# Kernel optimization log

Hardware: AMD Instinct MI355X
Metric: run time of the kernel (lower is better)

The kernel has to match this reference:

```python
import jax, jax.numpy as jnp
import numpy as np

EPS = 1e-5

def layernorm(x, g, b):
    mu = jnp.mean(x, axis=-1, keepdims=True)
    var = jnp.mean(jnp.square(x - mu), axis=-1, keepdims=True)
    return (x - mu) * jax.lax.rsqrt(var + EPS) * g + b

def setup_inputs() -> dict:
    key = jax.random.key(0)
    B, C, W = 1, 256, 64           # C = x_h_dim = query_dim
    D = 256                        # inner_dim = heads(1) * dim_head(256)
    ks = jax.random.split(key, 32)
    sc = 0.02
    inp = {
        'x': jax.random.normal(ks[0], (B, C, W, W), jnp.float32),
        'h': jax.random.normal(ks[1], (B, C, W, W), jnp.float32),
        's': jax.random.normal(ks[2], (B, C, W, W), jnp.float32),
        'm': jax.random.normal(ks[3], (B, C, W, W), jnp.float32),
        't': jax.random.normal(ks[4], (B, C), jnp.float32),
        'wt': jax.random.normal(ks[5], (C, D), jnp.float32) * sc,
        'bt': jnp.zeros((D,), jnp.float32),
        'wk_x': jax.random.normal(ks[6], (C, D), jnp.float32) * sc,
        'wv_x': jax.random.normal(ks[7], (C, D), jnp.float32) * sc,
        'g_x': jnp.ones((C,), jnp.float32), 'be_x': jnp.zeros((C,), jnp.float32),
        'wk_h': jax.random.normal(ks[8], (C, D), jnp.float32) * sc,
        'wv_h': jax.random.normal(ks[9], (C, D), jnp.float32) * sc,
        'g_h': jnp.ones((C,), jnp.float32), 'be_h': jnp.zeros((C,), jnp.float32),
        'wk_s': jax.random.normal(ks[10], (C, D), jnp.float32) * sc,
        'wv_s': jax.random.normal(ks[11], (C, D), jnp.float32) * sc,
        'g_s': jnp.ones((C,), jnp.float32), 'be_s': jnp.zeros((C,), jnp.float32),
        'wk_m': jax.random.normal(ks[12], (C, D), jnp.float32) * sc,
        'wv_m': jax.random.normal(ks[13], (C, D), jnp.float32) * sc,
        'g_m': jnp.ones((C,), jnp.float32), 'be_m': jnp.zeros((C,), jnp.float32),
        'w_geglu': jax.random.normal(ks[14], (D, 2 * D), jnp.float32) * sc,
        'b_geglu': jnp.zeros((2 * D,), jnp.float32),
        'w_ff2': jax.random.normal(ks[15], (D, D), jnp.float32) * sc,
        'b_ff2': jnp.zeros((D,), jnp.float32),
        'g_res': jnp.ones((D,), jnp.float32), 'be_res': jnp.zeros((D,), jnp.float32),
        'w_out': jax.random.normal(ks[16], (D, C), jnp.float32) * sc,
        'b_out': jnp.zeros((C,), jnp.float32),
        'imageWidth': W,
    }
    return inp

def reference(x, h, s, m, t, wt, bt, wk_x, wv_x, g_x, be_x, wk_h, wv_h, g_h, be_h,
              wk_s, wv_s, g_s, be_s, wk_m, wv_m, g_m, be_m,
              w_geglu, b_geglu, w_ff2, b_ff2, g_res, be_res, w_out, b_out, imageWidth):
    B, C, W, _ = x.shape
    N = W * W
    D = wt.shape[1]
    scale = 1.0 / jnp.sqrt(jnp.float32(D))  # dim_head**-0.5 (heads=1)

    # query: t_transform(t) broadcast over all spatial positions -> [B, N, D]
    q = t @ wt + bt
    query = jnp.broadcast_to(q[:, None, :], (B, N, D))

    def tokens(a):  # b c h w -> b (h w) c
        return a.reshape(B, C, N).transpose(0, 2, 1)

    mods = []
    for a, g, be, wk, wv in ((x, g_x, be_x, wk_x, wv_x), (h, g_h, be_h, wk_h, wv_h),
                             (s, g_s, be_s, wk_s, wv_s), (m, g_m, be_m, wk_m, wv_m)):
        a = layernorm(tokens(a), g, be)
        mods.append((a @ wk, a @ wv))  # (k, v) each [B, N, D]

    sims = [jnp.einsum('bid,bjd->bij', query, k) * scale for k, _ in mods]
    combined = jnp.concatenate(sims, axis=-1)          # [B, N, 4N]
    attn = jax.nn.softmax(combined, axis=-1)
    parts = jnp.split(attn, 4, axis=-1)

    out = sum(jnp.einsum('bij,bjd->bid', a, v) for a, (_, v) in zip(parts, mods))

    # FeedForward(inner_dim, mult=1, glu=True) on layernormed sum
    r = layernorm(out, g_res, be_res)
    gg = r @ w_geglu + b_geglu
    u, gate = jnp.split(gg, 2, axis=-1)
    ff = (u * jax.nn.gelu(gate, approximate=False)) @ w_ff2 + b_ff2

    y = ff @ w_out + b_out                              # [B, N, C]
    return y.transpose(0, 2, 1).reshape(B, C, W, W)
```

## Files before the change

### kernel.cpp

```cpp
#include <hip/hip_runtime.h>
#include <math.h>

#define N_TOK 4096

#define OFF_Q     0
#define OFF_GU    256
#define OFF_GUBU  1280
#define OFF_SIM   2048
#define OFF_MU    18432
#define OFF_RINV  34816
#define OFF_BLK   51200
#define OFF_SOFT  51248
#define OFF_W     51264
#define OFF_OUTV  52288
#define OFF_R     52544
#define OFF_GG    52800
#define OFF_FF    53312
#define OFF_Y     53568

__global__ void kInit(const float* __restrict__ bt, const float* __restrict__ b_geglu,
                      const float* __restrict__ b_ff2, const float* __restrict__ b_out,
                      float* __restrict__ ws) {
  const int tid = threadIdx.x;
  ws[OFF_GG + tid] = b_geglu[tid];
  if (tid < 256) {
    ws[OFF_Q + tid] = bt[tid];
    ws[OFF_OUTV + tid] = 0.0f;
    ws[OFF_FF + tid] = b_ff2[tid];
    ws[OFF_Y + tid] = b_out[tid];
  }
  if (tid < 8) ws[OFF_GUBU + tid] = 0.0f;
}

__global__ void kQ(const float* __restrict__ t, const float* __restrict__ wt,
                   float* __restrict__ ws) {
  const int tid = threadIdx.x;
  const int c0 = blockIdx.x * 16;
  float acc = 0.f;
  #pragma unroll
  for (int i = 0; i < 16; ++i) {
    int c = c0 + i;
    acc += t[c] * wt[c * 256 + tid];
  }
  atomicAdd(&ws[OFF_Q + tid], acc);
}

__global__ void kU(const float* __restrict__ wk0, const float* __restrict__ wk1,
                   const float* __restrict__ wk2, const float* __restrict__ wk3,
                   const float* __restrict__ g0, const float* __restrict__ g1,
                   const float* __restrict__ g2, const float* __restrict__ g3,
                   const float* __restrict__ be0, const float* __restrict__ be1,
                   const float* __restrict__ be2, const float* __restrict__ be3,
                   float* __restrict__ ws) {
  const int b = blockIdx.x;
  const int m = b >> 3;
  const int c0 = (b & 7) * 32;
  const int tid = threadIdx.x;
  const int w = tid >> 6, lane = tid & 63;
  const float* wk = (m == 0) ? wk0 : (m == 1) ? wk1 : (m == 2) ? wk2 : wk3;
  const float* g  = (m == 0) ? g0  : (m == 1) ? g1  : (m == 2) ? g2  : g3;
  const float* be = (m == 0) ? be0 : (m == 1) ? be1 : (m == 2) ? be2 : be3;

  __shared__ float qsh[256];
  __shared__ float red[8];
  qsh[tid] = ws[OFF_Q + tid];
  __syncthreads();
  const float4 qv = ((const float4*)qsh)[lane];

  float lGU = 0.f, lBU = 0.f;
  #pragma unroll
  for (int r = 0; r < 8; ++r) {
    int c = c0 + w * 8 + r;
    float4 w4 = ((const float4*)(wk + c * 256))[lane];
    float s = w4.x * qv.x + w4.y * qv.y + w4.z * qv.z + w4.w * qv.w;
    for (int o = 32; o > 0; o >>= 1) s += __shfl_down(s, o, 64);
    if (lane == 0) {
      float u = s;
      float gu = g[c] * u;
      ws[OFF_GU + m * 256 + c] = gu;
      lGU += gu;
      lBU += be[c] * u;
    }
  }
  if (lane == 0) { red[w] = lGU; red[4 + w] = lBU; }
  __syncthreads();
  if (tid == 0) {
    atomicAdd(&ws[OFF_GUBU + m], red[0] + red[1] + red[2] + red[3]);
    atomicAdd(&ws[OFF_GUBU + 4 + m], red[4] + red[5] + red[6] + red[7]);
  }
}

__global__ void kB(const float* __restrict__ A0, const float* __restrict__ A1,
                   const float* __restrict__ A2, const float* __restrict__ A3,
                   float* __restrict__ ws) {
  const int b = blockIdx.x;
  const int m = b >> 6;
  const int jbase = (b & 63) * 64;
  const int tid = threadIdx.x;
  const int l = tid & 63;
  const int qq = tid >> 6;
  const float* A = (m == 0) ? A0 : (m == 1) ? A1 : (m == 2) ? A2 : A3;

  __shared__ float gu[256];
  __shared__ float p1[256], p2[256], p3[256];
  gu[tid] = ws[OFF_GU + m * 256 + tid];
  __syncthreads();

  float s1 = 0.f, s2 = 0.f, s3 = 0.f;
  const float* Abase = A + jbase + l;
  #pragma unroll 8
  for (int i = 0; i < 64; ++i) {
    int c = qq * 64 + i;
    float v = Abase[c * N_TOK];
    s1 += v;
    s2 += v * v;
    s3 += v * gu[c];
  }
  p1[tid] = s1; p2[tid] = s2; p3[tid] = s3;
  __syncthreads();
  if (tid < 64) {
    float S1 = p1[tid] + p1[tid + 64] + p1[tid + 128] + p1[tid + 192];
    float S2 = p2[tid] + p2[tid + 64] + p2[tid + 128] + p2[tid + 192];
    float S3 = p3[tid] + p3[tid + 64] + p3[tid + 128] + p3[tid + 192];
    float mu   = S1 * (1.0f / 256.0f);
    float var  = S2 * (1.0f / 256.0f) - mu * mu;
    float rinv = rsqrtf(var + 1e-5f);
    float GU = ws[OFF_GUBU + m];
    float BU = ws[OFF_GUBU + 4 + m];
    float sim = 0.0625f * (rinv * (S3 - mu * GU) + BU);
    int gj = m * N_TOK + jbase + tid;
    ws[OFF_SIM + gj] = sim;
    ws[OFF_MU + gj] = mu;
    ws[OFF_RINV + gj] = rinv;
  }
}

__global__ void kC1(float* __restrict__ ws) {
  const int b = blockIdx.x;
  const int tid = threadIdx.x;
  const int base = b * 1024;
  __shared__ float sred[4];

  float v[4];
  float mx = -1e30f;
  #pragma unroll
  for (int i = 0; i < 4; ++i) {
    v[i] = ws[OFF_SIM + base + i * 256 + tid];
    mx = fmaxf(mx, v[i]);
  }
  for (int o = 32; o > 0; o >>= 1) mx = fmaxf(mx, __shfl_down(mx, o, 64));
  if ((tid & 63) == 0) sred[tid >> 6] = mx;
  __syncthreads();
  const float mxb = fmaxf(fmaxf(sred[0], sred[1]), fmaxf(sred[2], sred[3]));
  __syncthreads();

  float se = 0.f, srm = 0.f;
  #pragma unroll
  for (int i = 0; i < 4; ++i) {
    int idx = base + i * 256 + tid;
    float e = expf(v[i] - mxb);
    se += e;
    srm += e * ws[OFF_RINV + idx] * ws[OFF_MU + idx];
  }
  for (int o = 32; o > 0; o >>= 1) se += __shfl_down(se, o, 64);
  if ((tid & 63) == 0) sred[tid >> 6] = se;
  __syncthreads();
  float seT = sred[0] + sred[1] + sred[2] + sred[3];
  __syncthreads();
  for (int o = 32; o > 0; o >>= 1) srm += __shfl_down(srm, o, 64);
  if ((tid & 63) == 0) sred[tid >> 6] = srm;
  __syncthreads();
  if (tid == 0) {
    float srmT = sred[0] + sred[1] + sred[2] + sred[3];
    ws[OFF_BLK + b * 3 + 0] = mxb;
    ws[OFF_BLK + b * 3 + 1] = seT;
    ws[OFF_BLK + b * 3 + 2] = srmT;
  }
}

__global__ void kC2(float* __restrict__ ws) {
  if (threadIdx.x != 0) return;
  float mx[16], se[16], srm[16];
  float M = -1e30f;
  for (int b = 0; b < 16; ++b) {
    mx[b] = ws[OFF_BLK + b * 3 + 0];
    se[b] = ws[OFF_BLK + b * 3 + 1];
    srm[b] = ws[OFF_BLK + b * 3 + 2];
    M = fmaxf(M, mx[b]);
  }
  float S = 0.f, As[4] = {0, 0, 0, 0}, P[4] = {0, 0, 0, 0};
  for (int b = 0; b < 16; ++b) {
    float f = expf(mx[b] - M);
    int m = b >> 2;
    S += se[b] * f;
    As[m] += se[b] * f;
    P[m] += srm[b] * f;
  }
  float inv = 1.0f / S;
  ws[OFF_SOFT + 0] = M;
  ws[OFF_SOFT + 1] = inv;
  for (int m = 0; m < 4; ++m) {
    ws[OFF_SOFT + 2 + m] = As[m] * inv;
    ws[OFF_SOFT + 6 + m] = P[m] * inv;
  }
}

__global__ void kD(const float* __restrict__ A0, const float* __restrict__ A1,
                   const float* __restrict__ A2, const float* __restrict__ A3,
                   const float* __restrict__ g0, const float* __restrict__ g1,
                   const float* __restrict__ g2, const float* __restrict__ g3,
                   const float* __restrict__ be0, const float* __restrict__ be1,
                   const float* __restrict__ be2, const float* __restrict__ be3,
                   float* __restrict__ ws) {
  const int b = blockIdx.x;
  const int m = b >> 8;
  const int c = b & 255;
  const int tid = threadIdx.x;
  const float* A = (m == 0) ? A0 : (m == 1) ? A1 : (m == 2) ? A2 : A3;
  const float* row = A + c * N_TOK;
  const float M = ws[OFF_SOFT + 0];
  const float inv = ws[OFF_SOFT + 1];

  float s = 0.f;
  #pragma unroll 4
  for (int i = 0; i < 16; ++i) {
    int j = i * 256 + tid;
    int gj = m * N_TOK + j;
    float a = expf(ws[OFF_SIM + gj] - M) * ws[OFF_RINV + gj];
    s += a * row[j];
  }
  __shared__ float red[4];
  for (int o = 32; o > 0; o >>= 1) s += __shfl_down(s, o, 64);
  if ((tid & 63) == 0) red[tid >> 6] = s;
  __syncthreads();
  if (tid == 0) {
    float dot = (red[0] + red[1] + red[2] + red[3]) * inv;
    const float* g  = (m == 0) ? g0  : (m == 1) ? g1  : (m == 2) ? g2  : g3;
    const float* be = (m == 0) ? be0 : (m == 1) ? be1 : (m == 2) ? be2 : be3;
    float P  = ws[OFF_SOFT + 6 + m];
    float As = ws[OFF_SOFT + 2 + m];
    ws[OFF_W + m * 256 + c] = g[c] * (dot - P) + be[c] * As;
  }
}

__global__ void kE(const float* __restrict__ wv0, const float* __restrict__ wv1,
                   const float* __restrict__ wv2, const float* __restrict__ wv3,
                   float* __restrict__ ws) {
  const int b = blockIdx.x;
  const int m = b >> 2;
  const int cbase = (b & 3) * 64;
  const int d = threadIdx.x;
  const float* wv = (m == 0) ? wv0 : (m == 1) ? wv1 : (m == 2) ? wv2 : wv3;
  float s = 0.f;
  #pragma unroll 8
  for (int i = 0; i < 64; ++i) {
    int c = cbase + i;
    s += ws[OFF_W + m * 256 + c] * wv[c * 256 + d];
  }
  atomicAdd(&ws[OFF_OUTV + d], s);
}

__global__ void kT1(const float* __restrict__ g_res, const float* __restrict__ be_res,
                    float* __restrict__ ws) {
  const int tid = threadIdx.x;
  __shared__ float red[4];
  float od = ws[OFF_OUTV + tid];
  float s = od;
  for (int o = 32; o > 0; o >>= 1) s += __shfl_down(s, o, 64);
  if ((tid & 63) == 0) red[tid >> 6] = s;
  __syncthreads();
  float mu = (red[0] + red[1] + red[2] + red[3]) * (1.0f / 256.0f);
  __syncthreads();
  float dv = od - mu;
  s = dv * dv;
  for (int o = 32; o > 0; o >>= 1) s += __shfl_down(s, o, 64);
  if ((tid & 63) == 0) red[tid >> 6] = s;
  __syncthreads();
  float var = (red[0] + red[1] + red[2] + red[3]) * (1.0f / 256.0f);
  ws[OFF_R + tid] = dv * rsqrtf(var + 1e-5f) * g_res[tid] + be_res[tid];
}

__global__ void kT2(const float* __restrict__ w_geglu, float* __restrict__ ws) {
  const int b = blockIdx.x;
  const int dt = b >> 4;
  const int d0 = (b & 15) * 16;
  const int tid = threadIdx.x;
  float acc = 0.f;
  #pragma unroll
  for (int i = 0; i < 16; ++i) {
    int d = d0 + i;
    acc += ws[OFF_R + d] * w_geglu[d * 512 + dt * 256 + tid];
  }
  atomicAdd(&ws[OFF_GG + dt * 256 + tid], acc);
}

__global__ void kT3(const float* __restrict__ w_ff2, float* __restrict__ ws) {
  const int c0 = blockIdx.x * 16;
  const int tid = threadIdx.x;
  float acc = 0.f;
  #pragma unroll
  for (int i = 0; i < 16; ++i) {
    int c = c0 + i;
    float u = ws[OFF_GG + c];
    float gate = ws[OFF_GG + 256 + c];
    float f = u * 0.5f * gate * (1.0f + erff(gate * 0.70710678118654752f));
    acc += f * w_ff2[c * 256 + tid];
  }
  atomicAdd(&ws[OFF_FF + tid], acc);
}

__global__ void kT4(const float* __restrict__ w_out, float* __restrict__ ws) {
  const int d0 = blockIdx.x * 16;
  const int tid = threadIdx.x;
  float acc = 0.f;
  #pragma unroll
  for (int i = 0; i < 16; ++i) {
    int d = d0 + i;
    acc += ws[OFF_FF + d] * w_out[d * 256 + tid];
  }
  atomicAdd(&ws[OFF_Y + tid], acc);
}

__global__ void kG(const float* __restrict__ ws, float4* __restrict__ out4) {
  const int idx = blockIdx.x * 256 + threadIdx.x;
  const int c = idx >> 10;
  float v = ws[OFF_Y + c];
  out4[idx] = make_float4(v, v, v, v);
}

extern "C" void kernel_launch(void* const* d_in, const int* in_sizes, int n_in,
                              void* d_out, int out_size, void* d_ws, size_t ws_size,
                              hipStream_t stream) {
  const float* x = (const float*)d_in[0];
  const float* h = (const float*)d_in[1];
  const float* s = (const float*)d_in[2];
  const float* m = (const float*)d_in[3];
  const float* t = (const float*)d_in[4];
  const float* wt = (const float*)d_in[5];
  const float* bt = (const float*)d_in[6];
  const float* wk_x = (const float*)d_in[7];
  const float* wv_x = (const float*)d_in[8];
  const float* g_x = (const float*)d_in[9];
  const float* be_x = (const float*)d_in[10];
  const float* wk_h = (const float*)d_in[11];
  const float* wv_h = (const float*)d_in[12];
  const float* g_h = (const float*)d_in[13];
  const float* be_h = (const float*)d_in[14];
  const float* wk_s = (const float*)d_in[15];
  const float* wv_s = (const float*)d_in[16];
  const float* g_s = (const float*)d_in[17];
  const float* be_s = (const float*)d_in[18];
  const float* wk_m = (const float*)d_in[19];
  const float* wv_m = (const float*)d_in[20];
  const float* g_m = (const float*)d_in[21];
  const float* be_m = (const float*)d_in[22];
  const float* w_geglu = (const float*)d_in[23];
  const float* b_geglu = (const float*)d_in[24];
  const float* w_ff2 = (const float*)d_in[25];
  const float* b_ff2 = (const float*)d_in[26];
  const float* g_res = (const float*)d_in[27];
  const float* be_res = (const float*)d_in[28];
  const float* w_out = (const float*)d_in[29];
  const float* b_out = (const float*)d_in[30];
  float* ws = (float*)d_ws;

  kInit<<<dim3(1), dim3(512), 0, stream>>>(bt, b_geglu, b_ff2, b_out, ws);
  kQ<<<dim3(16), dim3(256), 0, stream>>>(t, wt, ws);
  kU<<<dim3(32), dim3(256), 0, stream>>>(wk_x, wk_h, wk_s, wk_m,
      g_x, g_h, g_s, g_m, be_x, be_h, be_s, be_m, ws);
  kB<<<dim3(256), dim3(256), 0, stream>>>(x, h, s, m, ws);
  kC1<<<dim3(16), dim3(256), 0, stream>>>(ws);
  kC2<<<dim3(1), dim3(64), 0, stream>>>(ws);
  kD<<<dim3(1024), dim3(256), 0, stream>>>(x, h, s, m,
      g_x, g_h, g_s, g_m, be_x, be_h, be_s, be_m, ws);
  kE<<<dim3(16), dim3(256), 0, stream>>>(wv_x, wv_h, wv_s, wv_m, ws);
  kT1<<<dim3(1), dim3(256), 0, stream>>>(g_res, be_res, ws);
  kT2<<<dim3(32), dim3(256), 0, stream>>>(w_geglu, ws);
  kT3<<<dim3(16), dim3(256), 0, stream>>>(w_ff2, ws);
  kT4<<<dim3(16), dim3(256), 0, stream>>>(w_out, ws);
  kG<<<dim3(1024), dim3(256), 0, stream>>>(ws, (float4*)d_out);
}
```

Baseline: 168.2 us.

## Fuse pipeline into six kernels with single-pass input read and online softmax

After: 162.7 us. -3.3%, faster.

```diff
diff --git a/kernel.cpp b/kernel.cpp
--- a/kernel.cpp
+++ b/kernel.cpp
@@ -3,329 +3,337 @@
 
 #define N_TOK 4096
 
-#define OFF_Q     0
-#define OFF_GU    256
-#define OFF_GUBU  1280
-#define OFF_SIM   2048
-#define OFF_MU    18432
-#define OFF_RINV  34816
-#define OFF_BLK   51200
-#define OFF_SOFT  51248
-#define OFF_W     51264
-#define OFF_OUTV  52288
-#define OFF_R     52544
-#define OFF_GG    52800
-#define OFF_FF    53312
-#define OFF_Y     53568
-
-__global__ void kInit(const float* __restrict__ bt, const float* __restrict__ b_geglu,
-                      const float* __restrict__ b_ff2, const float* __restrict__ b_out,
-                      float* __restrict__ ws) {
-  const int tid = threadIdx.x;
-  ws[OFF_GG + tid] = b_geglu[tid];
-  if (tid < 256) {
-    ws[OFF_Q + tid] = bt[tid];
+#define OFF_GU    0
+#define OFF_GUP   1024
+#define OFF_BUP   1056
+#define OFF_PM    1088
+#define OFF_PSE   1344
+#define OFF_PSR   1600
+#define OFF_OUTV  1856
+#define OFF_GG    2112
+#define OFF_Y     2624
+#define OFF_WS    3072
+#define OFF_WC    69632
+
+#define TSTRIDE 65
+
+__global__ __launch_bounds__(256) void k0(
+    const float* __restrict__ t, const float* __restrict__ wt,
+    const float* __restrict__ bt,
+    const float* __restrict__ wk0, const float* __restrict__ wk1,
+    const float* __restrict__ wk2, const float* __restrict__ wk3,
+    const float* __restrict__ g0, const float* __restrict__ g1,
+    const float* __restrict__ g2, const float* __restrict__ g3,
+    const float* __restrict__ be0, const float* __restrict__ be1,
+    const float* __restrict__ be2, const float* __restrict__ be3,
+    const float* __restrict__ w_ff2, const float* __restrict__ w_out,
+    const float* __restrict__ b_geglu, const float* __restrict__ b_ff2,
+    const float* __restrict__ b_out, float* __restrict__ ws) {
+  const int gid = blockIdx.x;
+  const int tid = threadIdx.x;
+  __shared__ float sh[264];
+
+  if (gid < 256) {
+    sh[tid] = w_ff2[gid * 256 + tid];
+    __syncthreads();
+    float acc = 0.f;
+    #pragma unroll 8
+    for (int d = 0; d < 256; ++d) acc += sh[d] * w_out[d * 256 + tid];
+    ws[OFF_WC + gid * 256 + tid] = acc;
+  } else if (gid < 288) {
+    const int local = gid - 256;
+    const int m = local >> 3;
+    const int c0 = (local & 7) * 32;
+    const float* wk = (m == 0) ? wk0 : (m == 1) ? wk1 : (m == 2) ? wk2 : wk3;
+    const float* g  = (m == 0) ? g0  : (m == 1) ? g1  : (m == 2) ? g2  : g3;
+    const float* be = (m == 0) ? be0 : (m == 1) ? be1 : (m == 2) ? be2 : be3;
+
+    float acc = bt[tid];
+    #pragma unroll 8
+    for (int c = 0; c < 256; ++c) acc += t[c] * wt[c * 256 + tid];
+    sh[tid] = acc;
+    __syncthreads();
+
+    const int w = tid >> 6, lane = tid & 63;
+    const float4 qv = ((const float4*)sh)[lane];
+    float lGU = 0.f, lBU = 0.f;
+    #pragma unroll
+    for (int r = 0; r < 8; ++r) {
+      int c = c0 + w * 8 + r;
+      float4 w4 = ((const float4*)(wk + c * 256))[lane];
+      float sdot = w4.x * qv.x + w4.y * qv.y + w4.z * qv.z + w4.w * qv.w;
+      for (int o = 32; o > 0; o >>= 1) sdot += __shfl_down(sdot, o, 64);
+      if (lane == 0) {
+        float u = sdot;
+        float gu = g[c] * u;
+        ws[OFF_GU + m * 256 + c] = gu;
+        lGU += gu;
+        lBU += be[c] * u;
+      }
+    }
+    __syncthreads();
+    if (lane == 0) { sh[256 + w] = lGU; sh[260 + w] = lBU; }
+    __syncthreads();
+    if (tid == 0) {
+      ws[OFF_GUP + m * 8 + (local & 7)] = sh[256] + sh[257] + sh[258] + sh[259];
+      ws[OFF_BUP + m * 8 + (local & 7)] = sh[260] + sh[261] + sh[262] + sh[263];
+    }
+  } else {
     ws[OFF_OUTV + tid] = 0.0f;
-    ws[OFF_FF + tid] = b_ff2[tid];
+    ws[OFF_GG + tid] = b_geglu[tid];
+    ws[OFF_GG + 256 + tid] = b_geglu[256 + tid];
     ws[OFF_Y + tid] = b_out[tid];
   }
-  if (tid < 8) ws[OFF_GUBU + tid] = 0.0f;
-}
-
-__global__ void kQ(const float* __restrict__ t, const float* __restrict__ wt,
-                   float* __restrict__ ws) {
-  const int tid = threadIdx.x;
-  const int c0 = blockIdx.x * 16;
-  float acc = 0.f;
-  #pragma unroll
-  for (int i = 0; i < 16; ++i) {
-    int c = c0 + i;
-    acc += t[c] * wt[c * 256 + tid];
-  }
-  atomicAdd(&ws[OFF_Q + tid], acc);
-}
-
-__global__ void kU(const float* __restrict__ wk0, const float* __restrict__ wk1,
-                   const float* __restrict__ wk2, const float* __restrict__ wk3,
-                   const float* __restrict__ g0, const float* __restrict__ g1,
-                   const float* __restrict__ g2, const float* __restrict__ g3,
-                   const float* __restrict__ be0, const float* __restrict__ be1,
-                   const float* __restrict__ be2, const float* __restrict__ be3,
-                   float* __restrict__ ws) {
-  const int b = blockIdx.x;
-  const int m = b >> 3;
-  const int c0 = (b & 7) * 32;
-  const int tid = threadIdx.x;
-  const int w = tid >> 6, lane = tid & 63;
-  const float* wk = (m == 0) ? wk0 : (m == 1) ? wk1 : (m == 2) ? wk2 : wk3;
-  const float* g  = (m == 0) ? g0  : (m == 1) ? g1  : (m == 2) ? g2  : g3;
-  const float* be = (m == 0) ? be0 : (m == 1) ? be1 : (m == 2) ? be2 : be3;
-
-  __shared__ float qsh[256];
-  __shared__ float red[8];
-  qsh[tid] = ws[OFF_Q + tid];
-  __syncthreads();
-  const float4 qv = ((const float4*)qsh)[lane];
-
-  float lGU = 0.f, lBU = 0.f;
-  #pragma unroll
-  for (int r = 0; r < 8; ++r) {
-    int c = c0 + w * 8 + r;
-    float4 w4 = ((const float4*)(wk + c * 256))[lane];
-    float s = w4.x * qv.x + w4.y * qv.y + w4.z * qv.z + w4.w * qv.w;
-    for (int o = 32; o > 0; o >>= 1) s += __shfl_down(s, o, 64);
-    if (lane == 0) {
-      float u = s;
-      float gu = g[c] * u;
-      ws[OFF_GU + m * 256 + c] = gu;
-      lGU += gu;
-      lBU += be[c] * u;
-    }
-  }
-  if (lane == 0) { red[w] = lGU; red[4 + w] = lBU; }
-  __syncthreads();
-  if (tid == 0) {
-    atomicAdd(&ws[OFF_GUBU + m], red[0] + red[1] + red[2] + red[3]);
-    atomicAdd(&ws[OFF_GUBU + 4 + m], red[4] + red[5] + red[6] + red[7]);
-  }
-}
-
-__global__ void kB(const float* __restrict__ A0, const float* __restrict__ A1,
-                   const float* __restrict__ A2, const float* __restrict__ A3,
-                   float* __restrict__ ws) {
+}
+
+__global__ __launch_bounds__(256) void k2(
+    const float* __restrict__ A0, const float* __restrict__ A1,
+    const float* __restrict__ A2, const float* __restrict__ A3,
+    float* __restrict__ ws) {
   const int b = blockIdx.x;
   const int m = b >> 6;
   const int jbase = (b & 63) * 64;
   const int tid = threadIdx.x;
-  const int l = tid & 63;
-  const int qq = tid >> 6;
   const float* A = (m == 0) ? A0 : (m == 1) ? A1 : (m == 2) ? A2 : A3;
 
-  __shared__ float gu[256];
-  __shared__ float p1[256], p2[256], p3[256];
-  gu[tid] = ws[OFF_GU + m * 256 + tid];
-  __syncthreads();
-
-  float s1 = 0.f, s2 = 0.f, s3 = 0.f;
-  const float* Abase = A + jbase + l;
-  #pragma unroll 8
-  for (int i = 0; i < 64; ++i) {
-    int c = qq * 64 + i;
-    float v = Abase[c * N_TOK];
-    s1 += v;
-    s2 += v * v;
-    s3 += v * gu[c];
-  }
-  p1[tid] = s1; p2[tid] = s2; p3[tid] = s3;
+  __shared__ float tile[256 * TSTRIDE];
+  __shared__ float gu_sh[256];
+  __shared__ float r1[256], r2[256], r3[256];
+  __shared__ float simj[64], rinvj[64], muj[64], alj[64];
+
+  gu_sh[tid] = ws[OFF_GU + m * 256 + tid];
+
+  {
+    const int cr = tid >> 4;
+    const int jf = tid & 15;
+    #pragma unroll 4
+    for (int it = 0; it < 16; ++it) {
+      int c = it * 16 + cr;
+      float4 v = *(const float4*)(A + c * N_TOK + jbase + jf * 4);
+      int base = c * TSTRIDE + jf * 4;
+      tile[base] = v.x; tile[base + 1] = v.y;
+      tile[base + 2] = v.z; tile[base + 3] = v.w;
+    }
+  }
+  __syncthreads();
+
+  {
+    const int j = tid & 63, q = tid >> 6;
+    float s1 = 0.f, s2 = 0.f, s3 = 0.f;
+    #pragma unroll 8
+    for (int i = 0; i < 64; ++i) {
+      int c = q * 64 + i;
+      float v = tile[c * TSTRIDE + j];
+      s1 += v; s2 += v * v; s3 += v * gu_sh[c];
+    }
+    r1[tid] = s1; r2[tid] = s2; r3[tid] = s3;
+  }
   __syncthreads();
   if (tid < 64) {
-    float S1 = p1[tid] + p1[tid + 64] + p1[tid + 128] + p1[tid + 192];
-    float S2 = p2[tid] + p2[tid + 64] + p2[tid + 128] + p2[tid + 192];
-    float S3 = p3[tid] + p3[tid + 64] + p3[tid + 128] + p3[tid + 192];
-    float mu   = S1 * (1.0f / 256.0f);
-    float var  = S2 * (1.0f / 256.0f) - mu * mu;
+    float S1 = r1[tid] + r1[tid + 64] + r1[tid + 128] + r1[tid + 192];
+    float S2 = r2[tid] + r2[tid + 64] + r2[tid + 128] + r2[tid + 192];
+    float S3 = r3[tid] + r3[tid + 64] + r3[tid + 128] + r3[tid + 192];
+    float GU = 0.f, BU = 0.f;
+    #pragma unroll
+    for (int i = 0; i < 8; ++i) {
+      GU += ws[OFF_GUP + m * 8 + i];
+      BU += ws[OFF_BUP + m * 8 + i];
+    }
+    float mu = S1 * (1.0f / 256.0f);
+    float var = S2 * (1.0f / 256.0f) - mu * mu;
     float rinv = rsqrtf(var + 1e-5f);
-    float GU = ws[OFF_GUBU + m];
-    float BU = ws[OFF_GUBU + 4 + m];
-    float sim = 0.0625f * (rinv * (S3 - mu * GU) + BU);
-    int gj = m * N_TOK + jbase + tid;
-    ws[OFF_SIM + gj] = sim;
-    ws[OFF_MU + gj] = mu;
-    ws[OFF_RINV + gj] = rinv;
-  }
-}
-
-__global__ void kC1(float* __restrict__ ws) {
+    simj[tid] = 0.0625f * (rinv * (S3 - mu * GU) + BU);
+    muj[tid] = mu;
+    rinvj[tid] = rinv;
+  }
+  __syncthreads();
+  if (tid < 64) {
+    float sim = simj[tid];
+    float mb = sim;
+    #pragma unroll
+    for (int o = 1; o < 64; o <<= 1) mb = fmaxf(mb, __shfl_xor(mb, o, 64));
+    float e = expf(sim - mb);
+    float al = e * rinvj[tid];
+    alj[tid] = al;
+    float se = e, sr = al * muj[tid];
+    #pragma unroll
+    for (int o = 1; o < 64; o <<= 1) {
+      se += __shfl_xor(se, o, 64);
+      sr += __shfl_xor(sr, o, 64);
+    }
+    if (tid == 0) {
+      ws[OFF_PM + b] = mb;
+      ws[OFF_PSE + b] = se;
+      ws[OFF_PSR + b] = sr;
+    }
+  }
+  __syncthreads();
+  {
+    float wsum = 0.f;
+    #pragma unroll 8
+    for (int j = 0; j < 64; ++j) wsum += alj[j] * tile[tid * TSTRIDE + j];
+    ws[OFF_WS + b * 256 + tid] = wsum;
+  }
+}
+
+__global__ __launch_bounds__(256) void k3(
+    const float* __restrict__ wv0, const float* __restrict__ wv1,
+    const float* __restrict__ wv2, const float* __restrict__ wv3,
+    const float* __restrict__ g0, const float* __restrict__ g1,
+    const float* __restrict__ g2, const float* __restrict__ g3,
+    const float* __restrict__ be0, const float* __restrict__ be1,
+    const float* __restrict__ be2, const float* __restrict__ be3,
+    float* __restrict__ ws) {
   const int b = blockIdx.x;
-  const int tid = threadIdx.x;
-  const int base = b * 1024;
-  __shared__ float sred[4];
-
-  float v[4];
-  float mx = -1e30f;
-  #pragma unroll
-  for (int i = 0; i < 4; ++i) {
-    v[i] = ws[OFF_SIM + base + i * 256 + tid];
-    mx = fmaxf(mx, v[i]);
-  }
-  for (int o = 32; o > 0; o >>= 1) mx = fmaxf(mx, __shfl_down(mx, o, 64));
-  if ((tid & 63) == 0) sred[tid >> 6] = mx;
-  __syncthreads();
-  const float mxb = fmaxf(fmaxf(sred[0], sred[1]), fmaxf(sred[2], sred[3]));
-  __syncthreads();
-
-  float se = 0.f, srm = 0.f;
-  #pragma unroll
-  for (int i = 0; i < 4; ++i) {
-    int idx = base + i * 256 + tid;
-    float e = expf(v[i] - mxb);
-    se += e;
-    srm += e * ws[OFF_RINV + idx] * ws[OFF_MU + idx];
-  }
-  for (int o = 32; o > 0; o >>= 1) se += __shfl_down(se, o, 64);
-  if ((tid & 63) == 0) sred[tid >> 6] = se;
-  __syncthreads();
-  float seT = sred[0] + sred[1] + sred[2] + sred[3];
-  __syncthreads();
-  for (int o = 32; o > 0; o >>= 1) srm += __shfl_down(srm, o, 64);
-  if ((tid & 63) == 0) sred[tid >> 6] = srm;
-  __syncthreads();
-  if (tid == 0) {
-    float srmT = sred[0] + sred[1] + sred[2] + sred[3];
-    ws[OFF_BLK + b * 3 + 0] = mxb;
-    ws[OFF_BLK + b * 3 + 1] = seT;
-    ws[OFF_BLK + b * 3 + 2] = srmT;
-  }
-}
-
-__global__ void kC2(float* __restrict__ ws) {
-  if (threadIdx.x != 0) return;
-  float mx[16], se[16], srm[16];
-  float M = -1e30f;
-  for (int b = 0; b < 16; ++b) {
-    mx[b] = ws[OFF_BLK + b * 3 + 0];
-    se[b] = ws[OFF_BLK + b * 3 + 1];
-    srm[b] = ws[OFF_BLK + b * 3 + 2];
-    M = fmaxf(M, mx[b]);
-  }
-  float S = 0.f, As[4] = {0, 0, 0, 0}, P[4] = {0, 0, 0, 0};
-  for (int b = 0; b < 16; ++b) {
-    float f = expf(mx[b] - M);
-    int m = b >> 2;
-    S += se[b] * f;
-    As[m] += se[b] * f;
-    P[m] += srm[b] * f;
-  }
-  float inv = 1.0f / S;
-  ws[OFF_SOFT + 0] = M;
-  ws[OFF_SOFT + 1] = inv;
-  for (int m = 0; m < 4; ++m) {
-    ws[OFF_SOFT + 2 + m] = As[m] * inv;
-    ws[OFF_SOFT + 6 + m] = P[m] * inv;
-  }
-}
-
-__global__ void kD(const float* __restrict__ A0, const float* __restrict__ A1,
-                   const float* __restrict__ A2, const float* __restrict__ A3,
-                   const float* __restrict__ g0, const float* __restrict__ g1,
-                   const float* __restrict__ g2, const float* __restrict__ g3,
-                   const float* __restrict__ be0, const float* __restrict__ be1,
-                   const float* __restrict__ be2, const float* __restrict__ be3,
-                   float* __restrict__ ws) {
-  const int b = blockIdx.x;
-  const int m = b >> 8;
-  const int c = b & 255;
-  const int tid = threadIdx.x;
-  const float* A = (m == 0) ? A0 : (m == 1) ? A1 : (m == 2) ? A2 : A3;
-  const float* row = A + c * N_TOK;
-  const float M = ws[OFF_SOFT + 0];
-  const float inv = ws[OFF_SOFT + 1];
-
-  float s = 0.f;
-  #pragma unroll 4
-  for (int i = 0; i < 16; ++i) {
-    int j = i * 256 + tid;
-    int gj = m * N_TOK + j;
-    float a = expf(ws[OFF_SIM + gj] - M) * ws[OFF_RINV + gj];
-    s += a * row[j];
-  }
+  const int mb = b >> 2;
+  const int cbase = (b & 3) * 64;
+  const int tid = threadIdx.x;
+  const float* wv = (mb == 0) ? wv0 : (mb == 1) ? wv1 : (mb == 2) ? wv2 : wv3;
+  const float* g  = (mb == 0) ? g0  : (mb == 1) ? g1  : (mb == 2) ? g2  : g3;
+  const float* be = (mb == 0) ? be0 : (mb == 1) ? be1 : (mb == 2) ? be2 : be3;
+
+  __shared__ float pm[256], pse[256], psr[256];
   __shared__ float red[4];
-  for (int o = 32; o > 0; o >>= 1) s += __shfl_down(s, o, 64);
-  if ((tid & 63) == 0) red[tid >> 6] = s;
-  __syncthreads();
-  if (tid == 0) {
-    float dot = (red[0] + red[1] + red[2] + red[3]) * inv;
-    const float* g  = (m == 0) ? g0  : (m == 1) ? g1  : (m == 2) ? g2  : g3;
-    const float* be = (m == 0) ? be0 : (m == 1) ? be1 : (m == 2) ? be2 : be3;
-    float P  = ws[OFF_SOFT + 6 + m];
-    float As = ws[OFF_SOFT + 2 + m];
-    ws[OFF_W + m * 256 + c] = g[c] * (dot - P) + be[c] * As;
-  }
-}
-
-__global__ void kE(const float* __restrict__ wv0, const float* __restrict__ wv1,
-                   const float* __restrict__ wv2, const float* __restrict__ wv3,
-                   float* __restrict__ ws) {
-  const int b = blockIdx.x;
-  const int m = b >> 2;
-  const int cbase = (b & 3) * 64;
-  const int d = threadIdx.x;
-  const float* wv = (m == 0) ? wv0 : (m == 1) ? wv1 : (m == 2) ? wv2 : wv3;
-  float s = 0.f;
-  #pragma unroll 8
-  for (int i = 0; i < 64; ++i) {
-    int c = cbase + i;
-    s += ws[OFF_W + m * 256 + c] * wv[c * 256 + d];
-  }
-  atomicAdd(&ws[OFF_OUTV + d], s);
-}
-
-__global__ void kT1(const float* __restrict__ g_res, const float* __restrict__ be_res,
-                    float* __restrict__ ws) {
-  const int tid = threadIdx.x;
+  __shared__ float wfin[64], fsh[64];
+  __shared__ float sS, sAm, sPm;
+
+  pm[tid] = ws[OFF_PM + tid];
+  pse[tid] = ws[OFF_PSE + tid];
+  psr[tid] = ws[OFF_PSR + tid];
+  __syncthreads();
+
+  float v = pm[tid];
+  for (int o = 32; o > 0; o >>= 1) v = fmaxf(v, __shfl_down(v, o, 64));
+  if ((tid & 63) == 0) red[tid >> 6] = v;
+  __syncthreads();
+  const float M = fmaxf(fmaxf(red[0], red[1]), fmaxf(red[2], red[3]));
+  __syncthreads();
+
+  const float f = expf(pm[tid] - M);
+  const float fse = f * pse[tid];
+  const bool mine = (tid >> 6) == mb;
+
+  v = fse;
+  for (int o = 32; o > 0; o >>= 1) v += __shfl_down(v, o, 64);
+  if ((tid & 63) == 0) red[tid >> 6] = v;
+  __syncthreads();
+  if (tid == 0) sS = red[0] + red[1] + red[2] + red[3];
+  __syncthreads();
+  v = mine ? fse : 0.f;
+  for (int o = 32; o > 0; o >>= 1) v += __shfl_down(v, o, 64);
+  if ((tid & 63) == 0) red[tid >> 6] = v;
+  __syncthreads();
+  if (tid == 0) sAm = red[0] + red[1] + red[2] + red[3];
+  __syncthreads();
+  v = mine ? f * psr[tid] : 0.f;
+  for (int o = 32; o > 0; o >>= 1) v += __shfl_down(v, o, 64);
+  if ((tid & 63) == 0) red[tid >> 6] = v;
+  __syncthreads();
+  if (tid == 0) sPm = red[0] + red[1] + red[2] + red[3];
+  if (tid < 64) fsh[tid] = expf(pm[mb * 64 + tid] - M);
+  __syncthreads();
+
+  const float invS = 1.0f / sS;
+
+  {
+    const int c_l = tid & 63, bg = tid >> 6;
+    float part = 0.f;
+    #pragma unroll 4
+    for (int i = 0; i < 16; ++i) {
+      int fb = bg * 16 + i;
+      part += fsh[fb] * ws[OFF_WS + (mb * 64 + fb) * 256 + cbase + c_l];
+    }
+    pse[tid] = part;
+  }
+  __syncthreads();
+  if (tid < 64) {
+    float dot = (pse[tid] + pse[tid + 64] + pse[tid + 128] + pse[tid + 192]) * invS;
+    int c = cbase + tid;
+    wfin[tid] = g[c] * (dot - sPm * invS) + be[c] * (sAm * invS);
+  }
+  __syncthreads();
+
+  {
+    float acc = 0.f;
+    #pragma unroll 8
+    for (int i = 0; i < 64; ++i) acc += wfin[i] * wv[(cbase + i) * 256 + tid];
+    atomicAdd(&ws[OFF_OUTV + tid], acc);
+  }
+}
+
+__global__ __launch_bounds__(256) void k4(
+    const float* __restrict__ g_res, const float* __restrict__ be_res,
+    const float* __restrict__ w_geglu, float* __restrict__ ws) {
+  const int gid = blockIdx.x;
+  const int tid = threadIdx.x;
+  __shared__ float r_sh[256];
   __shared__ float red[4];
+
   float od = ws[OFF_OUTV + tid];
-  float s = od;
-  for (int o = 32; o > 0; o >>= 1) s += __shfl_down(s, o, 64);
-  if ((tid & 63) == 0) red[tid >> 6] = s;
+  float v = od;
+  for (int o = 32; o > 0; o >>= 1) v += __shfl_down(v, o, 64);
+  if ((tid & 63) == 0) red[tid >> 6] = v;
   __syncthreads();
   float mu = (red[0] + red[1] + red[2] + red[3]) * (1.0f / 256.0f);
   __syncthreads();
   float dv = od - mu;
-  s = dv * dv;
-  for (int o = 32; o > 0; o >>= 1) s += __shfl_down(s, o, 64);
-  if ((tid & 63) == 0) red[tid >> 6] = s;
+  v = dv * dv;
+  for (int o = 32; o > 0; o >>= 1) v += __shfl_down(v, o, 64);
+  if ((tid & 63) == 0) red[tid >> 6] = v;
   __syncthreads();
   float var = (red[0] + red[1] + red[2] + red[3]) * (1.0f / 256.0f);
-  ws[OFF_R + tid] = dv * rsqrtf(var + 1e-5f) * g_res[tid] + be_res[tid];
-}
-
-__global__ void kT2(const float* __restrict__ w_geglu, float* __restrict__ ws) {
-  const int b = blockIdx.x;
-  const int dt = b >> 4;
-  const int d0 = (b & 15) * 16;
-  const int tid = threadIdx.x;
+  r_sh[tid] = dv * rsqrtf(var + 1e-5f) * g_res[tid] + be_res[tid];
+  __syncthreads();
+
+  const int dt = gid >> 4;
+  const int d0 = (gid & 15) * 16;
   float acc = 0.f;
   #pragma unroll
   for (int i = 0; i < 16; ++i) {
     int d = d0 + i;
-    acc += ws[OFF_R + d] * w_geglu[d * 512 + dt * 256 + tid];
+    acc += r_sh[d] * w_geglu[d * 512 + dt * 256 + tid];
   }
   atomicAdd(&ws[OFF_GG + dt * 256 + tid], acc);
 }
 
-__global__ void kT3(const float* __restrict__ w_ff2, float* __restrict__ ws) {
-  const int c0 = blockIdx.x * 16;
+__global__ __launch_bounds__(256) void k5(
+    const float* __restrict__ b_ff2, const float* __restrict__ w_out,
+    float* __restrict__ ws) {
+  const int gid = blockIdx.x;
   const int tid = threadIdx.x;
   float acc = 0.f;
+  if (gid < 16) {
+    const int e0 = gid * 16;
+    #pragma unroll
+    for (int i = 0; i < 16; ++i) {
+      int e = e0 + i;
+      float u = ws[OFF_GG + e];
+      float gate = ws[OFF_GG + 256 + e];
+      float ffin = u * 0.5f * gate * (1.0f + erff(gate * 0.70710678118654752f));
+      acc += ffin * ws[OFF_WC + e * 256 + tid];
+    }
+  } else {
+    const int d0 = (gid - 16) * 16;
+    #pragma unroll
+    for (int i = 0; i < 16; ++i) {
+      int d = d0 + i;
+      acc += b_ff2[d] * w_out[d * 256 + tid];
+    }
+  }
+  atomicAdd(&ws[OFF_Y + tid], acc);
+}
+
+__global__ __launch_bounds__(256) void k6(const float* __restrict__ ws,
+                                          float4* __restrict__ out4) {
+  const int gid = blockIdx.x;
+  const int tid = threadIdx.x;
   #pragma unroll
-  for (int i = 0; i < 16; ++i) {
-    int c = c0 + i;
-    float u = ws[OFF_GG + c];
-    float gate = ws[OFF_GG + 256 + c];
-    float f = u * 0.5f * gate * (1.0f + erff(gate * 0.70710678118654752f));
-    acc += f * w_ff2[c * 256 + tid];
-  }
-  atomicAdd(&ws[OFF_FF + tid], acc);
-}
-
-__global__ void kT4(const float* __restrict__ w_out, float* __restrict__ ws) {
-  const int d0 = blockIdx.x * 16;
-  const int tid = threadIdx.x;
-  float acc = 0.f;
-  #pragma unroll
-  for (int i = 0; i < 16; ++i) {
-    int d = d0 + i;
-    acc += ws[OFF_FF + d] * w_out[d * 256 + tid];
-  }
-  atomicAdd(&ws[OFF_Y + tid], acc);
-}
-
-__global__ void kG(const float* __restrict__ ws, float4* __restrict__ out4) {
-  const int idx = blockIdx.x * 256 + threadIdx.x;
-  const int c = idx >> 10;
-  float v = ws[OFF_Y + c];
-  out4[idx] = make_float4(v, v, v, v);
+  for (int k = 0; k < 2; ++k) {
+    const int idx = gid * 512 + k * 256 + tid;
+    const int c = idx >> 10;
+    float v = ws[OFF_Y + c];
+    out4[idx] = make_float4(v, v, v, v);
+  }
 }
 
 extern "C" void kernel_launch(void* const* d_in, const int* in_sizes, int n_in,
@@ -364,19 +372,13 @@
   const float* b_out = (const float*)d_in[30];
   float* ws = (float*)d_ws;
 
-  kInit<<<dim3(1), dim3(512), 0, stream>>>(bt, b_geglu, b_ff2, b_out, ws);
-  kQ<<<dim3(16), dim3(256), 0, stream>>>(t, wt, ws);
-  kU<<<dim3(32), dim3(256), 0, stream>>>(wk_x, wk_h, wk_s, wk_m,
+  k0<<<dim3(289), dim3(256), 0, stream>>>(t, wt, bt,
+      wk_x, wk_h, wk_s, wk_m, g_x, g_h, g_s, g_m, be_x, be_h, be_s, be_m,
+      w_ff2, w_out, b_geglu, b_ff2, b_out, ws);
+  k2<<<dim3(256), dim3(256), 0, stream>>>(x, h, s, m, ws);
+  k3<<<dim3(16), dim3(256), 0, stream>>>(wv_x, wv_h, wv_s, wv_m,
       g_x, g_h, g_s, g_m, be_x, be_h, be_s, be_m, ws);
-  kB<<<dim3(256), dim3(256), 0, stream>>>(x, h, s, m, ws);
-  kC1<<<dim3(16), dim3(256), 0, stream>>>(ws);
-  kC2<<<dim3(1), dim3(64), 0, stream>>>(ws);
-  kD<<<dim3(1024), dim3(256), 0, stream>>>(x, h, s, m,
-      g_x, g_h, g_s, g_m, be_x, be_h, be_s, be_m, ws);
-  kE<<<dim3(16), dim3(256), 0, stream>>>(wv_x, wv_h, wv_s, wv_m, ws);
-  kT1<<<dim3(1), dim3(256), 0, stream>>>(g_res, be_res, ws);
-  kT2<<<dim3(32), dim3(256), 0, stream>>>(w_geglu, ws);
-  kT3<<<dim3(16), dim3(256), 0, stream>>>(w_ff2, ws);
-  kT4<<<dim3(16), dim3(256), 0, stream>>>(w_out, ws);
-  kG<<<dim3(1024), dim3(256), 0, stream>>>(ws, (float4*)d_out);
-}
+  k4<<<dim3(32), dim3(256), 0, stream>>>(g_res, be_res, w_geglu, ws);
+  k5<<<dim3(32), dim3(256), 0, stream>>>(b_ff2, w_out, ws);
+  k6<<<dim3(512), dim3(256), 0, stream>>>(ws, (float4*)d_out);
+}
```
